# Performance work log

Hardware: AMD Instinct MI355X
Metric: run time of the kernel (lower is better)

The kernel has to match this reference:

```python
import jax, jax.numpy as jnp
import numpy as np

EPS = 1e-6
D_CONV = 4

def _layernorm(x):
    m = jnp.mean(x, axis=-1, keepdims=True)
    v = jnp.mean((x - m) ** 2, axis=-1, keepdims=True)
    return (x - m) / jnp.sqrt(v + EPS)

def setup_inputs() -> dict:
    key = jax.random.key(0)
    ks = jax.random.split(key, 20)
    B, L, D = 2, 4096, 1024
    Di = D          # expand = 1
    N = 16          # d_state
    R = 64          # dt_rank = ceil(D/16)
    H = 4 * D       # mlp hidden
    s = 0.02
    rn = lambda k, sh: s * jax.random.normal(k, sh, dtype=jnp.float32)
    x = jax.random.normal(ks[0], (B, L, D), dtype=jnp.float32)
    path = jax.random.permutation(ks[1], L).astype(jnp.int32)
    path_rev = jnp.argsort(path).astype(jnp.int32)
    A_log = jnp.log(jnp.tile(jnp.arange(1, N + 1, dtype=jnp.float32)[None, :], (Di, 1)))
    return {
        'x': x, 'path': path, 'path_rev': path_rev,
        'in_proj_w': rn(ks[2], (2 * Di, D)),
        'conv_w': rn(ks[3], (Di, D_CONV)), 'conv_b': rn(ks[4], (Di,)),
        'x_proj_w': rn(ks[5], (R + 2 * N, Di)),
        'dt_proj_w': rn(ks[6], (Di, R)), 'dt_proj_b': rn(ks[7], (Di,)),
        'A_log': A_log, 'D_param': jnp.ones((Di,), dtype=jnp.float32),
        'out_proj_w': rn(ks[8], (D, Di)),
        'fc1_w': rn(ks[9], (H, D)), 'fc1_b': jnp.zeros((H,), dtype=jnp.float32),
        'fc2_w': rn(ks[10], (D, H)), 'fc2_b': jnp.zeros((D,), dtype=jnp.float32),
    }

def _mamba(u, in_proj_w, conv_w, conv_b, x_proj_w, dt_proj_w, dt_proj_b, A_log, D_param, out_proj_w):
    B, L, _ = u.shape
    N = A_log.shape[1]
    R = dt_proj_w.shape[1]
    xz = u @ in_proj_w.T                      # (B,L,2*Di)
    xi, z = jnp.split(xz, 2, axis=-1)
    # causal depthwise conv1d, kernel 4
    xpad = jnp.pad(xi, ((0, 0), (D_CONV - 1, 0), (0, 0)))
    xc = conv_b + sum(conv_w[:, k] * xpad[:, k:k + L, :] for k in range(D_CONV))
    xc = jax.nn.silu(xc)                      # (B,L,Di)
    proj = xc @ x_proj_w.T                    # (B,L,R+2N)
    dt_r = proj[..., :R]
    Bm = proj[..., R:R + N]                   # (B,L,N)
    Cm = proj[..., R + N:]                    # (B,L,N)
    dt = jax.nn.softplus(dt_r @ dt_proj_w.T + dt_proj_b)  # (B,L,Di)
    A = -jnp.exp(A_log)                       # (Di,N)

    def step(h, inp):
        dt_t, B_t, C_t, x_t = inp             # (B,Di),(B,N),(B,N),(B,Di)
        dA = jnp.exp(dt_t[:, :, None] * A)    # (B,Di,N)
        h = dA * h + (dt_t * x_t)[:, :, None] * B_t[:, None, :]
        y = jnp.einsum('bdn,bn->bd', h, C_t)
        return h, y

    h0 = jnp.zeros((B, xc.shape[-1], N), dtype=u.dtype)
    xs = (dt.transpose(1, 0, 2), Bm.transpose(1, 0, 2), Cm.transpose(1, 0, 2), xc.transpose(1, 0, 2))
    _, ys = jax.lax.scan(step, h0, xs)        # (L,B,Di)
    y = ys.transpose(1, 0, 2) + D_param * xc
    y = y * jax.nn.silu(z)
    return y @ out_proj_w.T

def reference(x, path, path_rev, in_proj_w, conv_w, conv_b, x_proj_w, dt_proj_w, dt_proj_b,
              A_log, D_param, out_proj_w, fc1_w, fc1_b, fc2_w, fc2_b):
    tmp1 = x[:, path, :]                      # zigzag gather
    tmp1 = _mamba(_layernorm(tmp1), in_proj_w, conv_w, conv_b, x_proj_w,
                  dt_proj_w, dt_proj_b, A_log, D_param, out_proj_w)
    x = x + tmp1[:, path_rev, :]              # zigzag scatter (inverse gather)
    h = _layernorm(x)
    h = jax.nn.gelu(h @ fc1_w.T + fc1_b, approximate=True) @ fc2_w.T + fc2_b
    return x + h
```

## Files before the change

### kernel.cpp

```cpp
#include <hip/hip_runtime.h>
#include <cstdint>
#include <cstddef>

typedef unsigned short u16;
typedef __bf16 bf16x8 __attribute__((ext_vector_type(8)));
typedef float f32x4 __attribute__((ext_vector_type(4)));
typedef u16 u16x8 __attribute__((ext_vector_type(8)));

#define B_ 2
#define L_ 4096
#define D_ 1024
#define N_ 16
#define BL_ 8192
#define NC_ 64
#define LC_ 64

__device__ __forceinline__ float bf2f(u16 h) {
  union { unsigned int u; float f; } v; v.u = ((unsigned int)h) << 16; return v.f;
}
__device__ __forceinline__ u16 f2bf(float f) {
  union { float f; unsigned int u; } v; v.f = f;
  unsigned int r = v.u + 0x7FFFu + ((v.u >> 16) & 1u);
  return (u16)(r >> 16);
}
__device__ __forceinline__ float sigmoidf_(float x) { return 1.0f / (1.0f + __expf(-x)); }

#define WBF_TOT 11730944
__global__ __launch_bounds__(256) void cvt_w_k(
    const float* __restrict__ s0, const float* __restrict__ s1,
    const float* __restrict__ s2, const float* __restrict__ s3,
    const float* __restrict__ s4, const float* __restrict__ s5,
    u16* __restrict__ dst)
{
  int i = blockIdx.x * 256 + threadIdx.x;
  if (i >= WBF_TOT) return;
  float v;
  if (i < 2097152) v = s0[i];
  else if (i < 2228224) { int j = i - 2097152; v = (j < 98304) ? s1[j] : 0.0f; }
  else if (i < 2293760) v = s2[i - 2228224];
  else if (i < 3342336) v = s3[i - 2293760];
  else if (i < 7536640) v = s4[i - 3342336];
  else v = s5[i - 7536640];
  dst[i] = f2bf(v);
}

#define BK 32
enum { M_BF16 = 0, M_PROJ = 1, M_SOFTPLUS = 2, M_GELU = 3, M_BIASRES = 4, M_F32 = 5 };

#define GLDS(gp, lp) __builtin_amdgcn_global_load_lds( \
    (const __attribute__((address_space(1))) void*)(gp), \
    (__attribute__((address_space(3))) void*)(lp), 16, 0, 0)

template<int MODE>
__device__ __forceinline__ void epi_store(
    float v, size_t row, int col, int Nn,
    float* __restrict__ C, u16* __restrict__ C2,
    const float* __restrict__ bias, const u16* __restrict__ resid)
{
  if constexpr (MODE == M_BF16) {
    C2[row * Nn + col] = f2bf(v);
  } else if constexpr (MODE == M_PROJ) {
    C[row * 96 + col] = v;
    if (col < 64) C2[(row << 6) + col] = f2bf(v);
  } else if constexpr (MODE == M_SOFTPLUS) {
    v += bias[col];
    v = (v > 20.0f) ? v : log1pf(__expf(v));
    C2[row * Nn + col] = f2bf(v);
  } else if constexpr (MODE == M_GELU) {
    v += bias[col];
    float a = 0.7978845608028654f * (v + 0.044715f * v * v * v);
    float t = 1.0f - 2.0f / (__expf(2.0f * a) + 1.0f);
    C2[row * Nn + col] = f2bf(0.5f * v * (1.0f + t));
  } else if constexpr (MODE == M_BIASRES) {
    C[row * Nn + col] = v + bias[col] + bf2f(resid[row * Nn + col]);
  } else if constexpr (MODE == M_F32) {
    C[row * Nn + col] = v;
  }
}

#define BM 128
#define BN 128

template<int MODE, int K>
__global__ __launch_bounds__(256, 2) void gemm_bt(
    const u16* __restrict__ A, const u16* __restrict__ W,
    float* __restrict__ C, u16* __restrict__ C2,
    const float* __restrict__ bias, const u16* __restrict__ resid,
    int M, int N)
{
  __shared__ __align__(16) u16 As[3][BM * BK];
  __shared__ __align__(16) u16 Bs[3][BN * BK];

  const int id = blockIdx.x + gridDim.x * blockIdx.y;
  const int xcd = id & 7;
  const int qq = id >> 3;
  const int bandH = gridDim.y >> 3;
  const int xs = qq % gridDim.x;
  const int ys = xcd * bandH + qq / gridDim.x;
  const int bm = ys * BM;
  const int bn = xs * BN;

  const int tid = threadIdx.x;
  const int lane = tid & 63;
  const int wave = tid >> 6;
  const int wr = (wave >> 1) * 64;
  const int wc = (wave & 1) * 64;

  f32x4 acc[4][4];
#pragma unroll
  for (int i = 0; i < 4; ++i)
#pragma unroll
    for (int j = 0; j < 4; ++j)
#pragma unroll
      for (int r = 0; r < 4; ++r) acc[i][j][r] = 0.0f;

  const int r0 = tid >> 2;
  const int ke = (((tid & 3) ^ (r0 & 3)) << 3);
  const u16* Ab = A + (size_t)(bm + r0) * K + ke;
  const u16* Wb = W + (size_t)(bn + r0) * K + ke;
  constexpr size_t rstep = (size_t)64 * K;

  auto issue = [&](int buf, int k0) {
    GLDS(Ab + k0, &As[buf][tid * 8]);
    GLDS(Ab + k0 + rstep, &As[buf][(tid + 256) * 8]);
    GLDS(Wb + k0, &Bs[buf][tid * 8]);
    GLDS(Wb + k0 + rstep, &Bs[buf][(tid + 256) * 8]);
  };

  issue(0, 0);
  if constexpr (BK < K) issue(1, BK);

  const int mr = lane & 15;
  const int pos = (((lane >> 4) ^ (mr & 3)) << 3);
  constexpr int NIT = K / BK;

  auto step = [&](int it) {
    if (it + 1 < NIT) asm volatile("s_waitcnt vmcnt(4)" ::: "memory");
    else              asm volatile("s_waitcnt vmcnt(0)" ::: "memory");
    asm volatile("s_barrier" ::: "memory");
    if (it + 2 < NIT) issue((it + 2) % 3, (it + 2) * BK);
    const int cur = it % 3;
    bf16x8 af[4], bfr[4];
#pragma unroll
    for (int i = 0; i < 4; ++i)
      af[i] = *(const bf16x8*)(&As[cur][(wr + i * 16 + mr) * BK + pos]);
#pragma unroll
    for (int j = 0; j < 4; ++j)
      bfr[j] = *(const bf16x8*)(&Bs[cur][(wc + j * 16 + mr) * BK + pos]);
#pragma unroll
    for (int i = 0; i < 4; ++i)
#pragma unroll
      for (int j = 0; j < 4; ++j)
        acc[i][j] = __builtin_amdgcn_mfma_f32_16x16x32_bf16(af[i], bfr[j], acc[i][j], 0, 0, 0);
  };

  if constexpr (NIT <= 32) {
#pragma unroll
    for (int it = 0; it < NIT; ++it) step(it);
  } else {
#pragma unroll 6
    for (int it = 0; it < NIT; ++it) step(it);
  }

  const int mlo = (lane >> 4) << 2;
  const int nlo = lane & 15;
#pragma unroll
  for (int i = 0; i < 4; ++i) {
#pragma unroll
    for (int j = 0; j < 4; ++j) {
      int col = bn + wc + j * 16 + nlo;
      if (col < N) {
#pragma unroll
        for (int r = 0; r < 4; ++r) {
          size_t row = (size_t)(bm + wr + i * 16 + mlo + r);
          epi_store<MODE>(acc[i][j][r], row, col, N, C, C2, bias, resid);
        }
      }
    }
  }
}

#define P_MID asm volatile("s_barrier" ::: "memory")
#define P_END asm volatile("s_barrier" ::: "memory")
#define P_LG0 asm volatile("s_waitcnt lgkmcnt(0)" ::: "memory")
#define P_VM2 asm volatile("s_waitcnt vmcnt(2)" ::: "memory")
#define P_SB0 __builtin_amdgcn_sched_barrier(0)

#define PH(RD1, RD2, STG, MH, NH, VMW) \
  RD1; RD2; STG; \
  P_MID; P_LG0; P_SB0; \
  __builtin_amdgcn_s_setprio(1); mm(MH, NH); P_SB0; __builtin_amdgcn_s_setprio(0); \
  VMW; P_END;

template<int MODE, int KFULL, int KSPLIT>
__global__ __launch_bounds__(512, 2) void gemm256(
    const u16* __restrict__ A, const u16* __restrict__ W,
    float* __restrict__ C, u16* __restrict__ C2,
    const float* __restrict__ bias, const u16* __restrict__ resid,
    int M, int N)
{
  __shared__ __align__(16) u16 As[2][16384];
  __shared__ __align__(16) u16 Bs[2][16384];

  const int id = blockIdx.x + gridDim.x * blockIdx.y;
  const int xcd = id & 7;
  const int qq = id >> 3;
  const int bandH = gridDim.y >> 3;
  const int xs = qq % gridDim.x;
  const int ys = xcd * bandH + qq / gridDim.x;
  const int bm = ys * 256;
  const int bn = xs * 256;
  const int z = blockIdx.z;

  const int tid = threadIdx.x;
  const int lane = tid & 63;
  const int wave = tid >> 6;
  const int wm = (wave >> 2) * 128;
  const int wn = (wave & 3) * 64;
  const int mr = lane & 15;
  const int kq = lane >> 4;

  f32x4 acc[8][4];
#pragma unroll
  for (int i = 0; i < 8; ++i)
#pragma unroll
    for (int j = 0; j < 4; ++j)
#pragma unroll
      for (int r = 0; r < 4; ++r) acc[i][j][r] = 0.0f;

  const int row0 = tid >> 3;
  const int g = (tid & 7) ^ (row0 & 7);
  const u16* Asrc = A + (size_t)(bm + row0) * KFULL + (size_t)z * KSPLIT + g * 8;
  const u16* Wsrc = W + (size_t)(bn + row0) * KFULL + (size_t)z * KSPLIT + g * 8;

  auto stage = [&](int buf, int which , int T) {
    const int h = which & 1;
    const u16* s = ((which < 2) ? Asrc : Wsrc) + (size_t)(h * 128) * KFULL + T * 64;
    u16* d = (which < 2) ? &As[buf][h * 8192] : &Bs[buf][h * 8192];
    GLDS(s, d + tid * 8);
    GLDS(s + (size_t)64 * KFULL, d + (tid + 512) * 8);
  };

  bf16x8 Ar[8], Br[4];
  const int sl0 = ((kq ^ (mr & 7)) << 3);
  const int aB = (wm + mr) * 64;
  const int bB = (wn + mr) * 64;

  auto dsA = [&](int buf, int mh) {
#pragma unroll
    for (int i2 = 0; i2 < 4; ++i2) {
      Ar[i2 * 2 + 0] = *(const bf16x8*)&As[buf][aB + (mh * 4 + i2) * 1024 + sl0];
      Ar[i2 * 2 + 1] = *(const bf16x8*)&As[buf][aB + (mh * 4 + i2) * 1024 + (sl0 ^ 32)];
    }
  };
  auto dsB = [&](int buf, int nh) {
#pragma unroll
    for (int j2 = 0; j2 < 2; ++j2) {
      Br[j2 * 2 + 0] = *(const bf16x8*)&Bs[buf][bB + (nh * 2 + j2) * 1024 + sl0];
      Br[j2 * 2 + 1] = *(const bf16x8*)&Bs[buf][bB + (nh * 2 + j2) * 1024 + (sl0 ^ 32)];
    }
  };
  auto mm = [&](int mh, int nh) {
#pragma unroll
    for (int i2 = 0; i2 < 4; ++i2)
#pragma unroll
      for (int j2 = 0; j2 < 2; ++j2) {
        acc[mh * 4 + i2][nh * 2 + j2] = __builtin_amdgcn_mfma_f32_16x16x32_bf16(
            Ar[i2 * 2 + 0], Br[j2 * 2 + 0], acc[mh * 4 + i2][nh * 2 + j2], 0, 0, 0);
        acc[mh * 4 + i2][nh * 2 + j2] = __builtin_amdgcn_mfma_f32_16x16x32_bf16(
            Ar[i2 * 2 + 1], Br[j2 * 2 + 1], acc[mh * 4 + i2][nh * 2 + j2], 0, 0, 0);
      }
  };

  stage(0, 0, 0); stage(0, 1, 0); stage(0, 2, 0); stage(0, 3, 0);
  stage(1, 0, 1);
  P_VM2;
  asm volatile("s_barrier" ::: "memory");

  constexpr int NT = KSPLIT / 64;
  constexpr int NT2 = NT / 2;
#pragma unroll 1
  for (int t = 0; t < NT2; ++t) {
    const int T1 = 2 * t + 1, T2p = 2 * t + 2, T3 = 2 * t + 3;
    PH(dsA(0, 0), dsB(0, 0), stage(1, 1, T1), 0, 0, );
    PH(dsB(0, 1),          , stage(1, 2, T1), 0, 1, );
    PH(dsA(0, 1),          , stage(1, 3, T1), 1, 1, );
    PH(dsB(0, 0),          , stage(0, 0, T2p), 1, 0, P_VM2);
    PH(dsA(1, 0), dsB(1, 0), stage(0, 1, T2p), 0, 0, );
    PH(dsB(1, 1),          , stage(0, 2, T2p), 0, 1, );
    PH(dsA(1, 1),          , stage(0, 3, T2p), 1, 1, );
    PH(dsB(1, 0),          , stage(1, 0, T3), 1, 0, P_VM2);
  }
  asm volatile("s_waitcnt vmcnt(0)" ::: "memory");

  const int mlo = (lane >> 4) << 2;
  const int nlo = lane & 15;
  float* Cz = C;
  if constexpr (MODE == M_F32) Cz = C + (size_t)z * ((size_t)M * (size_t)N);
#pragma unroll
  for (int i = 0; i < 8; ++i)
#pragma unroll
    for (int j = 0; j < 4; ++j) {
      int col = bn + wn + j * 16 + nlo;
#pragma unroll
      for (int r = 0; r < 4; ++r) {
        size_t row = (size_t)(bm + wm + i * 16 + mlo + r);
        epi_store<MODE>(acc[i][j][r], row, col, N, Cz, C2, bias, resid);
      }
    }
}

__global__ __launch_bounds__(256) void fc2_comb_k(
    const float* __restrict__ p, const float* __restrict__ bias,
    const u16* __restrict__ resid, float* __restrict__ out)
{
  size_t i = ((((size_t)blockIdx.x << 8) + threadIdx.x) << 2);
  f32x4 a = *(const f32x4*)(p + i);
  f32x4 b = *(const f32x4*)(p + 8388608 + i);
  int col = (int)(i & 1023);
  f32x4 bs = *(const f32x4*)(bias + col);
  const u16* rr = resid + i;
  f32x4 o;
#pragma unroll
  for (int j = 0; j < 4; ++j) o[j] = a[j] + b[j] + bs[j] + bf2f(rr[j]);
  *(f32x4*)(out + i) = o;
}

__device__ __forceinline__ void blockReduce2(float& s, float& q) {
#pragma unroll
  for (int o = 32; o > 0; o >>= 1) { s += __shfl_down(s, o, 64); q += __shfl_down(q, o, 64); }
  __shared__ float red[2][4];
  int lane = threadIdx.x & 63, wave = threadIdx.x >> 6;
  if (lane == 0) { red[0][wave] = s; red[1][wave] = q; }
  __syncthreads();
  s = red[0][0] + red[0][1] + red[0][2] + red[0][3];
  q = red[1][0] + red[1][1] + red[1][2] + red[1][3];
}

__global__ __launch_bounds__(256) void ln_gather_k(
    const float* __restrict__ x, const int* __restrict__ path, u16* __restrict__ out)
{
  int b = blockIdx.x >> 12;
  int l = blockIdx.x & 4095;
  int src = path[l];
  const float* row = x + (((size_t)b * L_ + src) << 10);
  u16* orow = out + (((size_t)b * L_ + l) << 10);
  float v[4], s = 0.f, q = 0.f;
#pragma unroll
  for (int i = 0; i < 4; ++i) {
    v[i] = row[threadIdx.x + (i << 8)];
    s += v[i]; q += v[i] * v[i];
  }
  blockReduce2(s, q);
  float mean = s * (1.0f / 1024.0f);
  float var = q * (1.0f / 1024.0f) - mean * mean;
  float rstd = rsqrtf(var + 1e-6f);
#pragma unroll
  for (int i = 0; i < 4; ++i)
    orow[threadIdx.x + (i << 8)] = f2bf((v[i] - mean) * rstd);
}

__global__ __launch_bounds__(256) void ln_scatter_k(
    const float* __restrict__ x, const int* __restrict__ prev,
    const u16* __restrict__ mo, u16* __restrict__ xnew, u16* __restrict__ lnout)
{
  int b = blockIdx.x >> 12;
  int l = blockIdx.x & 4095;
  int pl = prev[l];
  const float* xr = x + (((size_t)b * L_ + l) << 10);
  const u16* mr_ = mo + (((size_t)b * L_ + pl) << 10);
  size_t base = ((size_t)blockIdx.x) << 10;
  float v[4], s = 0.f, q = 0.f;
#pragma unroll
  for (int i = 0; i < 4; ++i) {
    v[i] = xr[threadIdx.x + (i << 8)] + bf2f(mr_[threadIdx.x + (i << 8)]);
    s += v[i]; q += v[i] * v[i];
  }
  blockReduce2(s, q);
  float mean = s * (1.0f / 1024.0f);
  float var = q * (1.0f / 1024.0f) - mean * mean;
  float rstd = rsqrtf(var + 1e-6f);
#pragma unroll
  for (int i = 0; i < 4; ++i) {
    xnew[base + threadIdx.x + (i << 8)] = f2bf(v[i]);
    lnout[base + threadIdx.x + (i << 8)] = f2bf((v[i] - mean) * rstd);
  }
}

__global__ __launch_bounds__(256) void conv_silu_k(
    const u16* __restrict__ xz, const float* __restrict__ cw, const float* __restrict__ cb,
    u16* __restrict__ xc)
{
  int t = blockIdx.x * 256 + threadIdx.x;
  int d0 = (t & 127) << 3;
  int l  = (t >> 7) & 4095;
  int b  = t >> 19;
  float acc[8];
  f32x4 cb0 = *(const f32x4*)(&cb[d0]);
  f32x4 cb1 = *(const f32x4*)(&cb[d0 + 4]);
#pragma unroll
  for (int j = 0; j < 4; ++j) { acc[j] = cb0[j]; acc[4 + j] = cb1[j]; }
  f32x4 cwv[8];
#pragma unroll
  for (int j = 0; j < 8; ++j) cwv[j] = *(const f32x4*)(&cw[(d0 + j) << 2]);
#pragma unroll
  for (int k = 0; k < 4; ++k) {
    int ls = l + k - 3;
    if (ls >= 0) {
      u16x8 v = *(const u16x8*)(&xz[(((size_t)b * L_ + ls) << 11) + d0]);
#pragma unroll
      for (int j = 0; j < 8; ++j)
        acc[j] += cwv[j][k] * bf2f(v[j]);
    }
  }
  u16x8 o;
#pragma unroll
  for (int j = 0; j < 8; ++j) {
    float a = acc[j];
    a = a * sigmoidf_(a);
    o[j] = f2bf(a);
  }
  *(u16x8*)(&xc[(size_t)t << 3]) = o;
}

__global__ __launch_bounds__(256) void scan_p1_k(
    const u16* __restrict__ dt, const u16* __restrict__ xc, const float* __restrict__ proj,
    const float* __restrict__ A_log, float* __restrict__ acum, float* __restrict__ hloc)
{
  int c = blockIdx.x & (NC_ - 1);
  int q = (blockIdx.x >> 6) & 3;
  int b = blockIdx.x >> 8;
  int d = (q << 8) + threadIdx.x;
  float Arow[N_];
#pragma unroll
  for (int n = 0; n < N_; ++n) Arow[n] = -__expf(A_log[(d << 4) + n]);
  float h[N_], ac[N_];
#pragma unroll
  for (int n = 0; n < N_; ++n) { h[n] = 0.0f; ac[n] = 1.0f; }
  int l0 = c << 6;
  for (int i = 0; i < LC_; ++i) {
    size_t rowb = (size_t)b * L_ + (l0 + i);
    float dtv = bf2f(dt[(rowb << 10) + d]);
    float xv = bf2f(xc[(rowb << 10) + d]);
    float dtx = dtv * xv;
    const float* Bp = proj + rowb * 96 + 64;
#pragma unroll
    for (int n = 0; n < N_; ++n) {
      float dA = __expf(dtv * Arow[n]);
      h[n] = dA * h[n] + dtx * Bp[n];
      ac[n] *= dA;
    }
  }
  size_t sb = ((((size_t)b << 10) + d) << 10) + (c << 4);
#pragma unroll
  for (int n = 0; n < N_; ++n) { acum[sb + n] = ac[n]; hloc[sb + n] = h[n]; }
}

__global__ __launch_bounds__(256) void scan_p2_k(
    const float* __restrict__ acum, const float* __restrict__ hloc, float* __restrict__ hin)
{
  int idx = blockIdx.x * 256 + threadIdx.x;
  int n = idx & 15;
  int dn = idx >> 4;
  size_t base = ((size_t)dn << 10) + n;
  float hs = 0.0f;
  for (int c = 0; c < NC_; ++c) {
    hin[base + (c << 4)] = hs;
    hs = acum[base + (c << 4)] * hs + hloc[base + (c << 4)];
  }
}

__global__ __launch_bounds__(256) void scan_p3_k(
    const u16* __restrict__ dt, const u16* __restrict__ xc, const float* __restrict__ proj,
    const float* __restrict__ A_log, const float* __restrict__ Dp, const float* __restrict__ hin,
    const u16* __restrict__ xz, u16* __restrict__ yg)
{
  int c = blockIdx.x & (NC_ - 1);
  int q = (blockIdx.x >> 6) & 3;
  int b = blockIdx.x >> 8;
  int d = (q << 8) + threadIdx.x;
  float Arow[N_];
#pragma unroll
  for (int n = 0; n < N_; ++n) Arow[n] = -__expf(A_log[(d << 4) + n]);
  float h[N_];
  size_t sb = ((((size_t)b << 10) + d) << 10) + (c << 4);
#pragma unroll
  for (int n = 0; n < N_; ++n) h[n] = hin[sb + n];
  float Dv = Dp[d];
  int l0 = c << 6;
  for (int i = 0; i < LC_; ++i) {
    size_t rowb = (size_t)b * L_ + (l0 + i);
    float dtv = bf2f(dt[(rowb << 10) + d]);
    float xv = bf2f(xc[(rowb << 10) + d]);
    float dtx = dtv * xv;
    const float* Bp = proj + rowb * 96 + 64;
    const float* Cp = proj + rowb * 96 + 80;
    float y = 0.0f;
#pragma unroll
    for (int n = 0; n < N_; ++n) {
      float dA = __expf(dtv * Arow[n]);
      h[n] = dA * h[n] + dtx * Bp[n];
      y += h[n] * Cp[n];
    }
    y += Dv * xv;
    float zv = bf2f(xz[(rowb << 11) + 1024 + d]);
    yg[(rowb << 10) + d] = f2bf(y * zv * sigmoidf_(zv));
  }
}

extern "C" void kernel_launch(void* const* d_in, const int* in_sizes, int n_in,
                              void* d_out, int out_size, void* d_ws, size_t ws_size,
                              hipStream_t stream)
{
  const float* x_in      = (const float*)d_in[0];
  const int*   path      = (const int*)d_in[1];
  const int*   path_rev  = (const int*)d_in[2];
  const float* in_proj_w = (const float*)d_in[3];
  const float* conv_w    = (const float*)d_in[4];
  const float* conv_b    = (const float*)d_in[5];
  const float* x_proj_w  = (const float*)d_in[6];
  const float* dt_proj_w = (const float*)d_in[7];
  const float* dt_proj_b = (const float*)d_in[8];
  const float* A_log     = (const float*)d_in[9];
  const float* Dp        = (const float*)d_in[10];
  const float* out_pw    = (const float*)d_in[11];
  const float* fc1_w     = (const float*)d_in[12];
  const float* fc1_b     = (const float*)d_in[13];
  const float* fc2_w     = (const float*)d_in[14];
  const float* fc2_b     = (const float*)d_in[15];
  float* out = (float*)d_out;

  char* w = (char*)d_ws;
  size_t off = 0;
  auto alloc = [&](size_t bytes) -> char* {
    char* p = w + off;
    off = (off + bytes + 255) & ~(size_t)255;
    return p;
  };
  u16*   wbf   = (u16*)  alloc((size_t)WBF_TOT * 2);
  u16*   ln_bf = (u16*)  alloc((size_t)BL_ * 1024 * 2);
  u16*   xz    = (u16*)  alloc((size_t)BL_ * 2048 * 2);
  u16*   xc    = (u16*)  alloc((size_t)BL_ * 1024 * 2);
  char*  pool0 = alloc(0);
  float* proj  = (float*)alloc((size_t)BL_ * 96 * 4);
  u16*   dtr   = (u16*)  alloc((size_t)BL_ * 64 * 2);
  u16*   dt    = (u16*)  alloc((size_t)BL_ * 1024 * 2);
  float* acum  = (float*)alloc((size_t)2 * 1024 * NC_ * 16 * 4);
  float* hloc  = (float*)alloc((size_t)2 * 1024 * NC_ * 16 * 4);
  float* hin   = (float*)alloc((size_t)2 * 1024 * NC_ * 16 * 4);
  u16*   yg    = (u16*)  alloc((size_t)BL_ * 1024 * 2);
  u16*   h1b   = (u16*)pool0;
  off = (size_t)(pool0 - w) + ((size_t)BL_ * 4096 * 2);
  u16*   xnew  = (u16*)  alloc((size_t)BL_ * 1024 * 2);
  u16*   mo    = xz;
  float* pf    = (float*)ln_bf;

  const u16* w_inp = wbf;
  const u16* w_xp  = wbf + 2097152;
  const u16* w_dtp = wbf + 2228224;
  const u16* w_op  = wbf + 2293760;
  const u16* w_fc1 = wbf + 3342336;
  const u16* w_fc2 = wbf + 7536640;

  dim3 blk(256);
  dim3 blk5(512);
  cvt_w_k<<<WBF_TOT / 256, blk, 0, stream>>>(in_proj_w, x_proj_w, dt_proj_w, out_pw,
                                             fc1_w, fc2_w, wbf);
  ln_gather_k<<<BL_, blk, 0, stream>>>(x_in, path, ln_bf);
  gemm256<M_BF16, 1024, 1024><<<dim3(8, 32, 1), blk5, 0, stream>>>(ln_bf, w_inp, nullptr, xz, nullptr, nullptr, 8192, 2048);
  conv_silu_k<<<(BL_ * 128) / 256, blk, 0, stream>>>(xz, conv_w, conv_b, xc);
  gemm_bt<M_PROJ, 1024><<<dim3(1, 64), blk, 0, stream>>>(xc, w_xp, proj, dtr, nullptr, nullptr, 8192, 96);
  gemm_bt<M_SOFTPLUS, 64><<<dim3(8, 64), blk, 0, stream>>>(dtr, w_dtp, nullptr, dt, dt_proj_b, nullptr, 8192, 1024);
  scan_p1_k<<<2 * 4 * NC_, blk, 0, stream>>>(dt, xc, proj, A_log, acum, hloc);
  scan_p2_k<<<(2 * 1024 * 16) / 256, blk, 0, stream>>>(acum, hloc, hin);
  scan_p3_k<<<2 * 4 * NC_, blk, 0, stream>>>(dt, xc, proj, A_log, Dp, hin, xz, yg);
  gemm_bt<M_BF16, 1024><<<dim3(8, 64), blk, 0, stream>>>(yg, w_op, nullptr, mo, nullptr, nullptr, 8192, 1024);
  ln_scatter_k<<<BL_, blk, 0, stream>>>(x_in, path_rev, mo, xnew, ln_bf);
  gemm256<M_GELU, 1024, 1024><<<dim3(16, 32, 1), blk5, 0, stream>>>(ln_bf, w_fc1, nullptr, h1b, fc1_b, nullptr, 8192, 4096);
  gemm256<M_F32, 4096, 2048><<<dim3(4, 32, 2), blk5, 0, stream>>>(h1b, w_fc2, pf, nullptr, nullptr, nullptr, 8192, 1024);
  fc2_comb_k<<<8192, blk, 0, stream>>>(pf, fc2_b, xnew, out);
}
```

Measured before the change: 579.6 us.

## Restructure gemm256 pipeline to 4-stage K=32 ring buffer

```diff
diff --git a/kernel.cpp b/kernel.cpp
--- a/kernel.cpp
+++ b/kernel.cpp
@@ -180,18 +180,6 @@
   }
 }
 
-#define P_MID asm volatile("s_barrier" ::: "memory")
-#define P_END asm volatile("s_barrier" ::: "memory")
-#define P_LG0 asm volatile("s_waitcnt lgkmcnt(0)" ::: "memory")
-#define P_VM2 asm volatile("s_waitcnt vmcnt(2)" ::: "memory")
-#define P_SB0 __builtin_amdgcn_sched_barrier(0)
-
-#define PH(RD1, RD2, STG, MH, NH, VMW) \
-  RD1; RD2; STG; \
-  P_MID; P_LG0; P_SB0; \
-  __builtin_amdgcn_s_setprio(1); mm(MH, NH); P_SB0; __builtin_amdgcn_s_setprio(0); \
-  VMW; P_END;
-
 template<int MODE, int KFULL, int KSPLIT>
 __global__ __launch_bounds__(512, 2) void gemm256(
     const u16* __restrict__ A, const u16* __restrict__ W,
@@ -199,8 +187,8 @@
     const float* __restrict__ bias, const u16* __restrict__ resid,
     int M, int N)
 {
-  __shared__ __align__(16) u16 As[2][16384];
-  __shared__ __align__(16) u16 Bs[2][16384];
+  __shared__ __align__(16) u16 As[4][8192];
+  __shared__ __align__(16) u16 Bs[4][8192];
 
   const int id = blockIdx.x + gridDim.x * blockIdx.y;
   const int xcd = id & 7;
@@ -228,68 +216,54 @@
 #pragma unroll
       for (int r = 0; r < 4; ++r) acc[i][j][r] = 0.0f;
 
-  const int row0 = tid >> 3;
-  const int g = (tid & 7) ^ (row0 & 7);
+  const int row0 = tid >> 2;
+  const int g = (tid & 3) ^ (row0 & 3);
   const u16* Asrc = A + (size_t)(bm + row0) * KFULL + (size_t)z * KSPLIT + g * 8;
   const u16* Wsrc = W + (size_t)(bn + row0) * KFULL + (size_t)z * KSPLIT + g * 8;
 
-  auto stage = [&](int buf, int which , int T) {
-    const int h = which & 1;
-    const u16* s = ((which < 2) ? Asrc : Wsrc) + (size_t)(h * 128) * KFULL + T * 64;
-    u16* d = (which < 2) ? &As[buf][h * 8192] : &Bs[buf][h * 8192];
+  auto stage = [&](int buf, int isB, int T) {
+    const u16* s = (isB ? Wsrc : Asrc) + (size_t)T * 32;
+    u16* d = (isB ? &Bs[buf][0] : &As[buf][0]);
     GLDS(s, d + tid * 8);
-    GLDS(s + (size_t)64 * KFULL, d + (tid + 512) * 8);
+    GLDS(s + (size_t)128 * KFULL, d + (tid + 512) * 8);
   };
 
-  bf16x8 Ar[8], Br[4];
-  const int sl0 = ((kq ^ (mr & 7)) << 3);
-  const int aB = (wm + mr) * 64;
-  const int bB = (wn + mr) * 64;
-
-  auto dsA = [&](int buf, int mh) {
-#pragma unroll
-    for (int i2 = 0; i2 < 4; ++i2) {
-      Ar[i2 * 2 + 0] = *(const bf16x8*)&As[buf][aB + (mh * 4 + i2) * 1024 + sl0];
-      Ar[i2 * 2 + 1] = *(const bf16x8*)&As[buf][aB + (mh * 4 + i2) * 1024 + (sl0 ^ 32)];
-    }
-  };
-  auto dsB = [&](int buf, int nh) {
-#pragma unroll
-    for (int j2 = 0; j2 < 2; ++j2) {
-      Br[j2 * 2 + 0] = *(const bf16x8*)&Bs[buf][bB + (nh * 2 + j2) * 1024 + sl0];
-      Br[j2 * 2 + 1] = *(const bf16x8*)&Bs[buf][bB + (nh * 2 + j2) * 1024 + (sl0 ^ 32)];
-    }
-  };
-  auto mm = [&](int mh, int nh) {
-#pragma unroll
-    for (int i2 = 0; i2 < 4; ++i2)
-#pragma unroll
-      for (int j2 = 0; j2 < 2; ++j2) {
-        acc[mh * 4 + i2][nh * 2 + j2] = __builtin_amdgcn_mfma_f32_16x16x32_bf16(
-            Ar[i2 * 2 + 0], Br[j2 * 2 + 0], acc[mh * 4 + i2][nh * 2 + j2], 0, 0, 0);
-        acc[mh * 4 + i2][nh * 2 + j2] = __builtin_amdgcn_mfma_f32_16x16x32_bf16(
-            Ar[i2 * 2 + 1], Br[j2 * 2 + 1], acc[mh * 4 + i2][nh * 2 + j2], 0, 0, 0);
-      }
-  };
-
-  stage(0, 0, 0); stage(0, 1, 0); stage(0, 2, 0); stage(0, 3, 0);
-  stage(1, 0, 1);
-  P_VM2;
+  const int sl0 = ((kq ^ (mr & 3)) << 3);
+  const int aB = (wm + mr) * 32;
+  const int bB = (wn + mr) * 32;
+
+  stage(0, 0, 0); stage(0, 1, 0);
+  stage(1, 0, 1); stage(1, 1, 1);
+  stage(2, 0, 2); stage(2, 1, 2);
+  asm volatile("s_waitcnt vmcnt(8)" ::: "memory");
   asm volatile("s_barrier" ::: "memory");
 
-  constexpr int NT = KSPLIT / 64;
-  constexpr int NT2 = NT / 2;
+  constexpr int NT = KSPLIT / 32;
+  int cur = 0;
 #pragma unroll 1
-  for (int t = 0; t < NT2; ++t) {
-    const int T1 = 2 * t + 1, T2p = 2 * t + 2, T3 = 2 * t + 3;
-    PH(dsA(0, 0), dsB(0, 0), stage(1, 1, T1), 0, 0, );
-    PH(dsB(0, 1),          , stage(1, 2, T1), 0, 1, );
-    PH(dsA(0, 1),          , stage(1, 3, T1), 1, 1, );
-    PH(dsB(0, 0),          , stage(0, 0, T2p), 1, 0, P_VM2);
-    PH(dsA(1, 0), dsB(1, 0), stage(0, 1, T2p), 0, 0, );
-    PH(dsB(1, 1),          , stage(0, 2, T2p), 0, 1, );
-    PH(dsA(1, 1),          , stage(0, 3, T2p), 1, 1, );
-    PH(dsB(1, 0),          , stage(1, 0, T3), 1, 0, P_VM2);
+  for (int t = 0; t < NT; ++t) {
+    const int nxt = (cur + 3) & 3;
+    const u16* Abase = &As[cur][0];
+    const u16* Bbase = &Bs[cur][0];
+    bf16x8 Br[4], Ar[8];
+#pragma unroll
+    for (int j = 0; j < 4; ++j)
+      Br[j] = *(const bf16x8*)&Bbase[bB + j * 512 + sl0];
+#pragma unroll
+    for (int i = 0; i < 8; ++i)
+      Ar[i] = *(const bf16x8*)&Abase[aB + i * 512 + sl0];
+    stage(nxt, 0, t + 3);
+    stage(nxt, 1, t + 3);
+    __builtin_amdgcn_s_setprio(1);
+#pragma unroll
+    for (int i = 0; i < 8; ++i)
+#pragma unroll
+      for (int j = 0; j < 4; ++j)
+        acc[i][j] = __builtin_amdgcn_mfma_f32_16x16x32_bf16(Ar[i], Br[j], acc[i][j], 0, 0, 0);
+    __builtin_amdgcn_s_setprio(0);
+    asm volatile("s_waitcnt vmcnt(8)" ::: "memory");
+    asm volatile("s_barrier" ::: "memory");
+    cur = (cur + 1) & 3;
   }
   asm volatile("s_waitcnt vmcnt(0)" ::: "memory");
 
```

Result: no change. 569.2 us (-1.8%).

## Restructure 256x256 GEMM pipeline with interleaved wave tiles and deeper prefetch

Applied to the files above, without the earlier changes.

```diff
diff --git a/kernel.cpp b/kernel.cpp
--- a/kernel.cpp
+++ b/kernel.cpp
@@ -115,7 +115,7 @@
       for (int r = 0; r < 4; ++r) acc[i][j][r] = 0.0f;
 
   const int r0 = tid >> 2;
-  const int ke = (((tid & 3) ^ (r0 & 3)) << 3);
+  const int ke = (((tid & 3) ^ ((r0 >> 1) & 3)) << 3);
   const u16* Ab = A + (size_t)(bm + r0) * K + ke;
   const u16* Wb = W + (size_t)(bn + r0) * K + ke;
   constexpr size_t rstep = (size_t)64 * K;
@@ -131,7 +131,7 @@
   if constexpr (BK < K) issue(1, BK);
 
   const int mr = lane & 15;
-  const int pos = (((lane >> 4) ^ (mr & 3)) << 3);
+  const int pos = (((lane >> 4) ^ ((mr >> 1) & 3)) << 3);
   constexpr int NIT = K / BK;
 
   auto step = [&](int it) {
@@ -180,20 +180,8 @@
   }
 }
 
-#define P_MID asm volatile("s_barrier" ::: "memory")
-#define P_END asm volatile("s_barrier" ::: "memory")
-#define P_LG0 asm volatile("s_waitcnt lgkmcnt(0)" ::: "memory")
-#define P_VM2 asm volatile("s_waitcnt vmcnt(2)" ::: "memory")
-#define P_SB0 __builtin_amdgcn_sched_barrier(0)
-
-#define PH(RD1, RD2, STG, MH, NH, VMW) \
-  RD1; RD2; STG; \
-  P_MID; P_LG0; P_SB0; \
-  __builtin_amdgcn_s_setprio(1); mm(MH, NH); P_SB0; __builtin_amdgcn_s_setprio(0); \
-  VMW; P_END;
-
 template<int MODE, int KFULL, int KSPLIT>
-__global__ __launch_bounds__(512, 2) void gemm256(
+__global__ __launch_bounds__(512, 1) void gemm256(
     const u16* __restrict__ A, const u16* __restrict__ W,
     float* __restrict__ C, u16* __restrict__ C2,
     const float* __restrict__ bias, const u16* __restrict__ resid,
@@ -215,8 +203,8 @@
   const int tid = threadIdx.x;
   const int lane = tid & 63;
   const int wave = tid >> 6;
-  const int wm = (wave >> 2) * 128;
-  const int wn = (wave & 3) * 64;
+  const int wm = (wave >> 2) * 64;
+  const int wn2 = (wave & 3) * 32;
   const int mr = lane & 15;
   const int kq = lane >> 4;
 
@@ -235,29 +223,29 @@
 
   auto stage = [&](int buf, int which , int T) {
     const int h = which & 1;
-    const u16* s = ((which < 2) ? Asrc : Wsrc) + (size_t)(h * 128) * KFULL + T * 64;
-    u16* d = (which < 2) ? &As[buf][h * 8192] : &Bs[buf][h * 8192];
+    const u16* s = ((which < 2) ? Asrc : Wsrc) + (size_t)(h * 128) * KFULL + (size_t)T * 64;
+    u16* d = ((which < 2) ? &As[buf][0] : &Bs[buf][0]) + h * 8192;
     GLDS(s, d + tid * 8);
     GLDS(s + (size_t)64 * KFULL, d + (tid + 512) * 8);
   };
 
+  const int sl0 = ((kq ^ (mr & 7)) << 3);
+  const int aOff = (wm + mr) * 64;
+  const int bOff = (wn2 + mr) * 64;
+
   bf16x8 Ar[8], Br[4];
-  const int sl0 = ((kq ^ (mr & 7)) << 3);
-  const int aB = (wm + mr) * 64;
-  const int bB = (wn + mr) * 64;
-
-  auto dsA = [&](int buf, int mh) {
+  auto dsA = [&](const u16* base, int mh) {
 #pragma unroll
     for (int i2 = 0; i2 < 4; ++i2) {
-      Ar[i2 * 2 + 0] = *(const bf16x8*)&As[buf][aB + (mh * 4 + i2) * 1024 + sl0];
-      Ar[i2 * 2 + 1] = *(const bf16x8*)&As[buf][aB + (mh * 4 + i2) * 1024 + (sl0 ^ 32)];
-    }
-  };
-  auto dsB = [&](int buf, int nh) {
+      Ar[i2 * 2 + 0] = *(const bf16x8*)&base[mh * 8192 + aOff + i2 * 1024 + sl0];
+      Ar[i2 * 2 + 1] = *(const bf16x8*)&base[mh * 8192 + aOff + i2 * 1024 + (sl0 ^ 32)];
+    }
+  };
+  auto dsB = [&](const u16* base, int nh) {
 #pragma unroll
     for (int j2 = 0; j2 < 2; ++j2) {
-      Br[j2 * 2 + 0] = *(const bf16x8*)&Bs[buf][bB + (nh * 2 + j2) * 1024 + sl0];
-      Br[j2 * 2 + 1] = *(const bf16x8*)&Bs[buf][bB + (nh * 2 + j2) * 1024 + (sl0 ^ 32)];
+      Br[j2 * 2 + 0] = *(const bf16x8*)&base[nh * 8192 + bOff + j2 * 1024 + sl0];
+      Br[j2 * 2 + 1] = *(const bf16x8*)&base[nh * 8192 + bOff + j2 * 1024 + (sl0 ^ 32)];
     }
   };
   auto mm = [&](int mh, int nh) {
@@ -272,26 +260,49 @@
       }
   };
 
+#define BARR  asm volatile("s_barrier" ::: "memory")
+#define VMW6  asm volatile("s_waitcnt vmcnt(6)" ::: "memory")
+#define PRIO1 __builtin_amdgcn_s_setprio(1)
+#define PRIO0 __builtin_amdgcn_s_setprio(0)
+
   stage(0, 0, 0); stage(0, 1, 0); stage(0, 2, 0); stage(0, 3, 0);
-  stage(1, 0, 1);
-  P_VM2;
-  asm volatile("s_barrier" ::: "memory");
+  stage(1, 0, 1); stage(1, 3, 1); stage(1, 1, 1);
+  VMW6;
+  BARR;
 
   constexpr int NT = KSPLIT / 64;
-  constexpr int NT2 = NT / 2;
+  static_assert((NT & 1) == 0, "NT must be even");
 #pragma unroll 1
-  for (int t = 0; t < NT2; ++t) {
-    const int T1 = 2 * t + 1, T2p = 2 * t + 2, T3 = 2 * t + 3;
-    PH(dsA(0, 0), dsB(0, 0), stage(1, 1, T1), 0, 0, );
-    PH(dsB(0, 1),          , stage(1, 2, T1), 0, 1, );
-    PH(dsA(0, 1),          , stage(1, 3, T1), 1, 1, );
-    PH(dsB(0, 0),          , stage(0, 0, T2p), 1, 0, P_VM2);
-    PH(dsA(1, 0), dsB(1, 0), stage(0, 1, T2p), 0, 0, );
-    PH(dsB(1, 1),          , stage(0, 2, T2p), 0, 1, );
-    PH(dsA(1, 1),          , stage(0, 3, T2p), 1, 1, );
-    PH(dsB(1, 0),          , stage(1, 0, T3), 1, 0, P_VM2);
+  for (int tp = 0; tp < NT / 2; ++tp) {
+    {
+      const int Tn = 2 * tp + 1, Tnn = 2 * tp + 2;
+      dsA(As[0], 0); dsB(Bs[0], 0); stage(1, 2, Tn);
+      BARR; PRIO1; mm(0, 0); PRIO0; BARR;
+      dsB(Bs[0], 1);                stage(0, 0, Tnn);
+      BARR; PRIO1; mm(0, 1); PRIO0; BARR;
+      dsA(As[0], 1);                stage(0, 3, Tnn);
+      BARR; PRIO1; mm(1, 1); PRIO0; BARR;
+      dsB(Bs[0], 0);                stage(0, 1, Tnn);
+      BARR; PRIO1; mm(1, 0); PRIO0; VMW6; BARR;
+    }
+    {
+      const int Tn = 2 * tp + 2, Tnn = 2 * tp + 3;
+      dsA(As[1], 0); dsB(Bs[1], 0); stage(0, 2, Tn);
+      BARR; PRIO1; mm(0, 0); PRIO0; BARR;
+      dsB(Bs[1], 1);                stage(1, 0, Tnn);
+      BARR; PRIO1; mm(0, 1); PRIO0; BARR;
+      dsA(As[1], 1);                stage(1, 3, Tnn);
+      BARR; PRIO1; mm(1, 1); PRIO0; BARR;
+      dsB(Bs[1], 0);                stage(1, 1, Tnn);
+      BARR; PRIO1; mm(1, 0); PRIO0; VMW6; BARR;
+    }
   }
   asm volatile("s_waitcnt vmcnt(0)" ::: "memory");
+
+#undef BARR
+#undef VMW6
+#undef PRIO1
+#undef PRIO0
 
   const int mlo = (lane >> 4) << 2;
   const int nlo = lane & 15;
@@ -301,10 +312,10 @@
   for (int i = 0; i < 8; ++i)
 #pragma unroll
     for (int j = 0; j < 4; ++j) {
-      int col = bn + wn + j * 16 + nlo;
+      int col = bn + (j >> 1) * 128 + wn2 + (j & 1) * 16 + nlo;
 #pragma unroll
       for (int r = 0; r < 4; ++r) {
-        size_t row = (size_t)(bm + wm + i * 16 + mlo + r);
+        size_t row = (size_t)(bm + (i >> 2) * 128 + wm + (i & 3) * 16 + mlo + r);
         epi_store<MODE>(acc[i][j][r], row, col, N, Cz, C2, bias, resid);
       }
     }
```

Result: no change. 580.5 us (+0.2%).
